# Performance work log

Measured on AMD Instinct MI355X. Metric: run time of the kernel, lower is better.

## Reference

```python
import jax, jax.numpy as jnp
import numpy as np

M_DIM = 256  # attention key dim, used for 1/sqrt(M) scaling


def sparsemax(z):
    # z: [..., F]. Martins & Astudillo sparsemax along last axis.
    F = z.shape[-1]
    zs = -jnp.sort(-z, axis=-1)                      # sorted descending
    css = jnp.cumsum(zs, axis=-1)                    # cumulative sums
    r = jnp.arange(1, F + 1, dtype=z.dtype)
    support = zs * r > (css - 1.0)                   # k(z) condition
    k = jnp.sum(support, axis=-1, keepdims=True)     # support size >= 1
    css_k = jnp.take_along_axis(css, k.astype(jnp.int32) - 1, axis=-1)
    tau = (css_k - 1.0) / k.astype(z.dtype)          # threshold
    return jnp.maximum(z - tau, 0.0)


def setup_inputs() -> dict:
    key = jax.random.key(0)
    ks = jax.random.split(key, 5)
    B, D, F, M = 4096, 1024, 8192, M_DIM
    bound = 0.01
    x = jax.random.normal(ks[0], (B, D), dtype=jnp.float32)
    X_data = jax.random.normal(ks[1], (F, D), dtype=jnp.float32)
    Wq = jax.random.uniform(ks[2], (M, D), dtype=jnp.float32, minval=-bound, maxval=bound)
    Wk = jax.random.uniform(ks[3], (M, D), dtype=jnp.float32, minval=-bound, maxval=bound)
    Wv = jax.random.uniform(ks[4], (D, D), dtype=jnp.float32, minval=-2 * bound, maxval=2 * bound)
    return {
        'x': x, 'X_data': X_data,
        'Wq': Wq, 'bq': jnp.zeros((M,), jnp.float32),
        'Wk': Wk, 'bk': jnp.zeros((M,), jnp.float32),
        'Wv': Wv, 'bv': jnp.zeros((D,), jnp.float32),
    }


def reference(x, X_data, Wq, bq, Wk, bk, Wv, bv):
    M = Wq.shape[0]
    scale = 1.0 / jnp.sqrt(jnp.asarray(M, x.dtype))
    Q = (x @ Wq.T + bq) * scale            # [B, M]
    K = (X_data @ Wk.T + bk) * scale       # [F, M]
    V = X_data @ Wv.T + bv                 # [F, D]
    scores = Q @ K.T                       # [B, F]  (note: 1/M total scaling, as in source)
    attn = sparsemax(scores)               # [B, F], sparse simplex projection
    x_hat = attn @ V                       # [B, D]
    return (x, x_hat, attn)
```

## Files before the change

kernel.cpp:

```cpp
#include <hip/hip_runtime.h>
#include <cstdint>
#include <cstddef>

typedef __attribute__((ext_vector_type(4))) float f32x4;
typedef __attribute__((ext_vector_type(8))) short bf16x8;
typedef __attribute__((ext_vector_type(4))) unsigned short u16x4;
typedef __attribute__((ext_vector_type(8))) unsigned short u16x8;

#define GPTR(p) ((const __attribute__((address_space(1))) void*)(p))
#define LPTR(p) ((__attribute__((address_space(3))) void*)(p))

static constexpr int BB = 4096;
static constexpr int DD = 1024;
static constexpr int FF = 8192;
static constexpr int MM = 256;

__device__ __forceinline__ unsigned short f2bf(float f) {
    union { float f; unsigned u; } x; x.f = f;
    return (unsigned short)((x.u + 0x7FFFu + ((x.u >> 16) & 1u)) >> 16);
}
__device__ __forceinline__ float bf2f(unsigned short h) {
    union { unsigned u; float f; } x; x.u = ((unsigned)h) << 16;
    return x.f;
}
__device__ __forceinline__ int xcd_swz(int bid, int grid) {
    const int cpx = grid >> 3;
    return (bid & 7) * cpx + (bid >> 3);
}

__global__ __launch_bounds__(256) void cvt_all(
    const float* __restrict__ x,  const float* __restrict__ Xd,
    const float* __restrict__ Wq, const float* __restrict__ Wk, const float* __restrict__ Wv,
    float* __restrict__ out_x,
    unsigned short* __restrict__ xb,  unsigned short* __restrict__ Xb,
    unsigned short* __restrict__ Wqb, unsigned short* __restrict__ Wkb, unsigned short* __restrict__ Wvb)
{
    constexpr int S0 = BB * DD;
    constexpr int S1 = FF * DD;
    constexpr int SW = MM * DD;
    const int i = (blockIdx.x * 256 + threadIdx.x) * 4;
    if (i < S0) {
        f32x4 v = *(const f32x4*)(x + i);
        *(f32x4*)(out_x + i) = v;
        u16x4 o; o.x = f2bf(v.x); o.y = f2bf(v.y); o.z = f2bf(v.z); o.w = f2bf(v.w);
        *(u16x4*)(xb + i) = o;
    } else if (i < S0 + S1) {
        const int j = i - S0;
        f32x4 v = *(const f32x4*)(Xd + j);
        u16x4 o; o.x = f2bf(v.x); o.y = f2bf(v.y); o.z = f2bf(v.z); o.w = f2bf(v.w);
        *(u16x4*)(Xb + j) = o;
    } else {
        int j = i - S0 - S1;
        const float* in; unsigned short* outp;
        if (j < SW)            { in = Wq; outp = Wqb; }
        else if (j < 2 * SW)   { in = Wk; outp = Wkb; j -= SW; }
        else                   { in = Wv; outp = Wvb; j -= 2 * SW; }
        f32x4 v = *(const f32x4*)(in + j);
        u16x4 o; o.x = f2bf(v.x); o.y = f2bf(v.y); o.z = f2bf(v.z); o.w = f2bf(v.w);
        *(u16x4*)(outp + j) = o;
    }
}

template<int Mo, int No, int Kd, int BIAS_MODE>
__device__ __forceinline__ void gemm128_core(
    const unsigned short* __restrict__ A,
    const unsigned short* __restrict__ Bm,
    unsigned short* __restrict__ Out,
    const float* __restrict__ bias, float scale,
    int L, unsigned short* As, unsigned short* Bs)
{
    constexpr int mt = Mo >> 7, nt = No >> 7;
    const int tid  = threadIdx.x;
    const int lane = tid & 63;
    const int wid  = tid >> 6;
    const int tm = (L % mt) << 7;
    const int tn = ((L / mt) % nt) << 7;
    const int wm = (wid >> 1) * 64;
    const int wn = (wid & 1) * 64;
    const int lr = lane & 15;
    const int lg = lane >> 4;

    f32x4 acc[4][4] = {};

    const unsigned short* aptr = A  + (size_t)(tm + (tid >> 2)) * Kd + ((tid & 3) << 3);
    const unsigned short* bptr = Bm + (size_t)(tn + (tid >> 2)) * Kd + ((tid & 3) << 3);
    unsigned short* As_base = &As[wid * 512];
    unsigned short* Bs_base = &Bs[wid * 512];

    for (int k0 = 0; k0 < Kd; k0 += 32) {
        __builtin_amdgcn_global_load_lds(GPTR(aptr + k0),                   LPTR(As_base),        16, 0, 0);
        __builtin_amdgcn_global_load_lds(GPTR(aptr + (size_t)64 * Kd + k0), LPTR(As_base + 2048), 16, 0, 0);
        __builtin_amdgcn_global_load_lds(GPTR(bptr + k0),                   LPTR(Bs_base),        16, 0, 0);
        __builtin_amdgcn_global_load_lds(GPTR(bptr + (size_t)64 * Kd + k0), LPTR(Bs_base + 2048), 16, 0, 0);
        __syncthreads();

        bf16x8 af[4], bfr[4];
        #pragma unroll
        for (int mi = 0; mi < 4; ++mi)
            af[mi] = *(const bf16x8*)&As[(wm + mi * 16 + lr) * 32 + lg * 8];
        #pragma unroll
        for (int ni = 0; ni < 4; ++ni)
            bfr[ni] = *(const bf16x8*)&Bs[(wn + ni * 16 + lr) * 32 + lg * 8];

        #pragma unroll
        for (int mi = 0; mi < 4; ++mi)
            #pragma unroll
            for (int ni = 0; ni < 4; ++ni)
                acc[mi][ni] = __builtin_amdgcn_mfma_f32_16x16x32_bf16(af[mi], bfr[ni], acc[mi][ni], 0, 0, 0);
        __syncthreads();
    }

    #pragma unroll
    for (int mi = 0; mi < 4; ++mi)
        #pragma unroll
        for (int ni = 0; ni < 4; ++ni)
            #pragma unroll
            for (int r = 0; r < 4; ++r) {
                const int row = tm + wm + mi * 16 + lg * 4 + r;
                const int col = tn + wn + ni * 16 + lr;
                float v = acc[mi][ni][r];
                if (BIAS_MODE == 1) v = (v + bias[col]) * scale;
                if (BIAS_MODE == 2) v = v + bias[row];
                Out[(size_t)row * No + col] = f2bf(v);
            }
}

__global__ __launch_bounds__(256) void proj_all(
    const unsigned short* __restrict__ xb,  const unsigned short* __restrict__ Xb,
    const unsigned short* __restrict__ Wqb, const unsigned short* __restrict__ Wkb,
    const unsigned short* __restrict__ Wvb,
    unsigned short* __restrict__ Qb, unsigned short* __restrict__ Kb, unsigned short* __restrict__ Vtb,
    const float* __restrict__ bq, const float* __restrict__ bk, const float* __restrict__ bv,
    float scl)
{
    __shared__ alignas(16) unsigned short As[128 * 32];
    __shared__ alignas(16) unsigned short Bs[128 * 32];
    const int bid = blockIdx.x;
    if (bid < 512) {
        gemm128_core<DD, FF, DD, 2>(Wvb, Xb, Vtb, bv, 1.0f, xcd_swz(bid, 512), As, Bs);
    } else if (bid < 640) {
        gemm128_core<FF, MM, DD, 1>(Xb, Wkb, Kb, bk, scl, xcd_swz(bid - 512, 128), As, Bs);
    } else {
        gemm128_core<BB, MM, DD, 1>(xb, Wqb, Qb, bq, scl, xcd_swz(bid - 640, 64), As, Bs);
    }
}

template<int Mo, int No, int Kd, int KC, int DIRECT>
__global__ __launch_bounds__(512) void gemm256(
    const unsigned short* __restrict__ A,
    const unsigned short* __restrict__ Bm,
    unsigned short* __restrict__ Out)
{
    constexpr int KCH = Kd / KC;
    constexpr int NT  = KCH / 32;
    constexpr int mt  = Mo >> 8;
    constexpr int nt  = No >> 8;

    __shared__ alignas(16) unsigned short SH[4 * 16384];

    const int tid  = threadIdx.x;
    const int lane = tid & 63;
    const int wid  = tid >> 6;
    const int wr   = wid >> 2;
    const int wc   = wid & 3;
    const int lr   = lane & 15;
    const int lg   = lane >> 4;

    const int L  = xcd_swz(blockIdx.x, KC * mt * nt);
    const int tn = (L % nt) << 8;
    const int r0 = L / nt;
    const int tm = (r0 % mt) << 8;
    const int kc = r0 / mt;
    const size_t kbase = (size_t)kc * KCH;

    const unsigned short* ag0 = A  + (size_t)(tm + (tid >> 2)) * Kd + kbase + ((tid & 3) << 3);
    const unsigned short* bg0 = Bm + (size_t)(tn + (tid >> 2)) * Kd + kbase + ((tid & 3) << 3);

    auto STAGE_A = [&](int tt) {
        const int buf = tt & 3;
        #pragma unroll
        for (int s = 0; s < 2; ++s)
            __builtin_amdgcn_global_load_lds(GPTR(ag0 + (size_t)(s * 128) * Kd + tt * 32),
                LPTR(&SH[buf * 16384 + s * 4096 + wid * 512]), 16, 0, 0);
    };
    auto STAGE_B = [&](int tt) {
        const int buf = tt & 3;
        #pragma unroll
        for (int s = 0; s < 2; ++s)
            __builtin_amdgcn_global_load_lds(GPTR(bg0 + (size_t)(s * 128) * Kd + tt * 32),
                LPTR(&SH[buf * 16384 + 8192 + s * 4096 + wid * 512]), 16, 0, 0);
    };

    f32x4 acc[8][4] = {};

    STAGE_A(0); STAGE_B(0);
    STAGE_A(1); STAGE_B(1);
    STAGE_A(2); STAGE_B(2);
    asm volatile("s_waitcnt vmcnt(8)" ::: "memory");
    __builtin_amdgcn_s_barrier();

    #pragma unroll 1
    for (int t = 0; t < NT; ++t) {
        if (t) {
            if (t < NT - 2)      asm volatile("s_waitcnt vmcnt(8)" ::: "memory");
            else if (t == NT-2)  asm volatile("s_waitcnt vmcnt(4)" ::: "memory");
            else                 asm volatile("s_waitcnt vmcnt(0)" ::: "memory");
            __builtin_amdgcn_s_barrier();
        }
        const int buf = t & 3;
        const unsigned short* Ab = &SH[buf * 16384];
        const unsigned short* Bb = &SH[buf * 16384 + 8192];

        bf16x8 bfr[4], af[4];
        #pragma unroll
        for (int ni = 0; ni < 4; ++ni)
            bfr[ni] = *(const bf16x8*)&Bb[(wc * 64 + ni * 16 + lr) * 32 + lg * 8];
        #pragma unroll
        for (int mi = 0; mi < 4; ++mi)
            af[mi] = *(const bf16x8*)&Ab[(wr * 128 + mi * 16 + lr) * 32 + lg * 8];
        if (t + 3 < NT) STAGE_A(t + 3);
        __builtin_amdgcn_sched_barrier(0);
        __builtin_amdgcn_s_setprio(1);
        #pragma unroll
        for (int mi = 0; mi < 4; ++mi)
            #pragma unroll
            for (int ni = 0; ni < 4; ++ni)
                acc[mi][ni] = __builtin_amdgcn_mfma_f32_16x16x32_bf16(af[mi], bfr[ni], acc[mi][ni], 0, 0, 0);
        __builtin_amdgcn_s_setprio(0);
        __builtin_amdgcn_s_barrier();

        bf16x8 af2[4];
        #pragma unroll
        for (int mi = 0; mi < 4; ++mi)
            af2[mi] = *(const bf16x8*)&Ab[(wr * 128 + 64 + mi * 16 + lr) * 32 + lg * 8];
        if (t + 3 < NT) STAGE_B(t + 3);
        __builtin_amdgcn_sched_barrier(0);
        __builtin_amdgcn_s_setprio(1);
        #pragma unroll
        for (int mi = 0; mi < 4; ++mi)
            #pragma unroll
            for (int ni = 0; ni < 4; ++ni)
                acc[4 + mi][ni] = __builtin_amdgcn_mfma_f32_16x16x32_bf16(af2[mi], bfr[ni], acc[4 + mi][ni], 0, 0, 0);
        __builtin_amdgcn_s_setprio(0);
    }

    unsigned short* Ok = DIRECT ? (Out + (size_t)tm * No + tn)
                                : (Out + ((size_t)kc * Mo + tm) * No + tn);
    #pragma unroll
    for (int mi = 0; mi < 8; ++mi)
        #pragma unroll
        for (int ni = 0; ni < 4; ++ni)
            #pragma unroll
            for (int r = 0; r < 4; ++r) {
                const int row = wr * 128 + mi * 16 + lg * 4 + r;
                const int col = wc * 64 + ni * 16 + lr;
                Ok[(size_t)row * No + col] = f2bf(acc[mi][ni][r]);
            }
}

template<int KC>
__global__ __launch_bounds__(256) void reduce_sk(
    const unsigned short* __restrict__ P, float* __restrict__ out, size_t total)
{
    const size_t i = ((size_t)blockIdx.x * 256 + threadIdx.x) * 8;
    float v[8] = {0,0,0,0,0,0,0,0};
    #pragma unroll
    for (int kc = 0; kc < KC; ++kc) {
        u16x8 p = *(const u16x8*)(P + kc * total + i);
        #pragma unroll
        for (int c = 0; c < 8; ++c) v[c] += bf2f(p[c]);
    }
    f32x4 o0, o1;
    #pragma unroll
    for (int c = 0; c < 4; ++c) { o0[c] = v[c]; o1[c] = v[4 + c]; }
    *(f32x4*)(out + i)     = o0;
    *(f32x4*)(out + i + 4) = o1;
}

__global__ __launch_bounds__(256) void sparsemax_k(unsigned short* __restrict__ SA,
                                                   float* __restrict__ attn)
{
    __shared__ float red[16];
    const int t = threadIdx.x;
    const int w = t >> 6, lane = t & 63;
    unsigned short* Zrow = SA + (size_t)blockIdx.x * FF;
    float* Arow = attn + (size_t)blockIdx.x * FF;

    f32x4 z[8];
    #pragma unroll
    for (int j = 0; j < 4; ++j) {
        u16x8 v = *(const u16x8*)&Zrow[j * 2048 + t * 8];
        #pragma unroll
        for (int c = 0; c < 4; ++c) {
            z[2 * j][c]     = bf2f(v[c]);
            z[2 * j + 1][c] = bf2f(v[4 + c]);
        }
    }

    float mx = -1e30f, sm = 0.0f;
    #pragma unroll
    for (int j = 0; j < 8; ++j)
        #pragma unroll
        for (int c = 0; c < 4; ++c) { mx = fmaxf(mx, z[j][c]); sm += z[j][c]; }
    #pragma unroll
    for (int off = 32; off > 0; off >>= 1) {
        mx = fmaxf(mx, __shfl_xor(mx, off));
        sm += __shfl_xor(sm, off);
    }
    if (lane == 0) { red[w] = mx; red[8 + w] = sm; }
    __syncthreads();
    mx = fmaxf(fmaxf(red[0], red[1]), fmaxf(red[2], red[3]));
    sm = red[8] + red[9] + red[10] + red[11];
    __syncthreads();

    float lo = fmaxf(mx - 1.0f, (sm - 1.0f) * (1.0f / (float)FF));
    float hi = mx - 1.0f / (float)FF;

    for (int it = 0; it < 8; ++it) {
        const float mid = 0.5f * (lo + hi);
        float s = 0.0f;
        #pragma unroll
        for (int j = 0; j < 8; ++j)
            #pragma unroll
            for (int c = 0; c < 4; ++c) s += fmaxf(z[j][c] - mid, 0.0f);
        #pragma unroll
        for (int off = 32; off > 0; off >>= 1) s += __shfl_xor(s, off);
        if (lane == 0) red[w] = s;
        __syncthreads();
        s = red[0] + red[1] + red[2] + red[3];
        __syncthreads();
        if (s >= 1.0f) lo = mid; else hi = mid;
    }

    for (int it = 0; it < 2; ++it) {
        float s = 0.0f, cnt = 0.0f;
        #pragma unroll
        for (int j = 0; j < 8; ++j)
            #pragma unroll
            for (int c = 0; c < 4; ++c) {
                const float v = z[j][c];
                if (v > lo) { s += v; cnt += 1.0f; }
            }
        #pragma unroll
        for (int off = 32; off > 0; off >>= 1) { s += __shfl_xor(s, off); cnt += __shfl_xor(cnt, off); }
        if (lane == 0) { red[w] = s; red[8 + w] = cnt; }
        __syncthreads();
        s   = red[0] + red[1] + red[2] + red[3];
        cnt = red[8] + red[9] + red[10] + red[11];
        __syncthreads();
        lo = (s - 1.0f) / cnt;
    }
    const float tau = lo;

    #pragma unroll
    for (int j = 0; j < 4; ++j) {
        f32x4 a0, a1;
        #pragma unroll
        for (int c = 0; c < 4; ++c) {
            a0[c] = fmaxf(z[2 * j][c] - tau, 0.0f);
            a1[c] = fmaxf(z[2 * j + 1][c] - tau, 0.0f);
        }
        *(f32x4*)&Arow[j * 2048 + t * 8]     = a0;
        *(f32x4*)&Arow[j * 2048 + t * 8 + 4] = a1;
        u16x8 o;
        #pragma unroll
        for (int c = 0; c < 4; ++c) { o[c] = f2bf(a0[c]); o[4 + c] = f2bf(a1[c]); }
        *(u16x8*)&Zrow[j * 2048 + t * 8] = o;
    }
}

extern "C" void kernel_launch(void* const* d_in, const int* in_sizes, int n_in,
                              void* d_out, int out_size, void* d_ws, size_t ws_size,
                              hipStream_t stream) {
    const float* x  = (const float*)d_in[0];
    const float* Xd = (const float*)d_in[1];
    const float* Wq = (const float*)d_in[2];
    const float* bq = (const float*)d_in[3];
    const float* Wk = (const float*)d_in[4];
    const float* bk = (const float*)d_in[5];
    const float* Wv = (const float*)d_in[6];
    const float* bv = (const float*)d_in[7];

    float* out       = (float*)d_out;
    float* out_xhat  = out + (size_t)BB * DD;
    float* out_attn  = out + (size_t)2 * BB * DD;

    char* w = (char*)d_ws;
    unsigned short* xb  = (unsigned short*)w; w += (size_t)BB * DD * 2;
    unsigned short* Xb  = (unsigned short*)w; w += (size_t)FF * DD * 2;
    unsigned short* Wqb = (unsigned short*)w; w += (size_t)MM * DD * 2;
    unsigned short* Wkb = (unsigned short*)w; w += (size_t)MM * DD * 2;
    unsigned short* Wvb = (unsigned short*)w; w += (size_t)DD * DD * 2;
    unsigned short* Qb  = (unsigned short*)w; w += (size_t)BB * MM * 2;
    unsigned short* Kb  = (unsigned short*)w; w += (size_t)FF * MM * 2;
    unsigned short* Vtb = (unsigned short*)w; w += (size_t)DD * FF * 2;
    unsigned short* Sb  = (unsigned short*)w; w += (size_t)BB * FF * 2;

    unsigned short* Pb = (unsigned short*)d_ws;

    constexpr int CVT_N = BB * DD + FF * DD + 2 * MM * DD + DD * DD;
    cvt_all<<<CVT_N / 1024, 256, 0, stream>>>(x, Xd, Wq, Wk, Wv, out, xb, Xb, Wqb, Wkb, Wvb);

    proj_all<<<704, 256, 0, stream>>>(xb, Xb, Wqb, Wkb, Wvb, Qb, Kb, Vtb, bq, bk, bv, 0.0625f);

    gemm256<BB, FF, MM, 1, 1><<<(BB/256) * (FF/256), 512, 0, stream>>>(Qb, Kb, Sb);

    sparsemax_k<<<BB, 256, 0, stream>>>(Sb, out_attn);

    gemm256<BB, DD, FF, 4, 0><<<4 * (BB/256) * (DD/256), 512, 0, stream>>>(Sb, Vtb, Pb);

    reduce_sk<4><<<BB * DD / 2048, 256, 0, stream>>>(Pb, out_xhat, (size_t)BB * DD);
}
```

Baseline: 214.7 us.

## Co-schedule V projection GEMM with sparsemax in one launch

Moves the V projection GEMM out of the initial projection launch and fuses it into the same grid as the row-wise sparsemax, so the compute-bound GEMM blocks and the memory-bound sparsemax blocks can run concurrently on the GPU. The Q/K projection launch shrinks to 192 blocks, so the scores GEMM can start earlier. The fused kernel carries both the GEMM shared-memory footprint and the reduction buffer, and the small Q/K launch may underfill the device.

```diff
diff --git a/kernel.cpp b/kernel.cpp
--- a/kernel.cpp
+++ b/kernel.cpp
@@ -125,23 +125,125 @@
             }
 }
 
-__global__ __launch_bounds__(256) void proj_all(
+__global__ __launch_bounds__(256) void proj_qk(
     const unsigned short* __restrict__ xb,  const unsigned short* __restrict__ Xb,
     const unsigned short* __restrict__ Wqb, const unsigned short* __restrict__ Wkb,
-    const unsigned short* __restrict__ Wvb,
-    unsigned short* __restrict__ Qb, unsigned short* __restrict__ Kb, unsigned short* __restrict__ Vtb,
-    const float* __restrict__ bq, const float* __restrict__ bk, const float* __restrict__ bv,
-    float scl)
+    unsigned short* __restrict__ Qb, unsigned short* __restrict__ Kb,
+    const float* __restrict__ bq, const float* __restrict__ bk, float scl)
 {
     __shared__ alignas(16) unsigned short As[128 * 32];
     __shared__ alignas(16) unsigned short Bs[128 * 32];
     const int bid = blockIdx.x;
+    if (bid < 128) {
+        gemm128_core<FF, MM, DD, 1>(Xb, Wkb, Kb, bk, scl, xcd_swz(bid, 128), As, Bs);
+    } else {
+        gemm128_core<BB, MM, DD, 1>(xb, Wqb, Qb, bq, scl, xcd_swz(bid - 128, 64), As, Bs);
+    }
+}
+
+__device__ __forceinline__ void sparsemax_row(unsigned short* __restrict__ Zrow,
+                                              float* __restrict__ Arow, float* red)
+{
+    const int t = threadIdx.x;
+    const int w = t >> 6, lane = t & 63;
+
+    f32x4 z[8];
+    #pragma unroll
+    for (int j = 0; j < 4; ++j) {
+        u16x8 v = *(const u16x8*)&Zrow[j * 2048 + t * 8];
+        #pragma unroll
+        for (int c = 0; c < 4; ++c) {
+            z[2 * j][c]     = bf2f(v[c]);
+            z[2 * j + 1][c] = bf2f(v[4 + c]);
+        }
+    }
+
+    float mx = -1e30f, sm = 0.0f;
+    #pragma unroll
+    for (int j = 0; j < 8; ++j)
+        #pragma unroll
+        for (int c = 0; c < 4; ++c) { mx = fmaxf(mx, z[j][c]); sm += z[j][c]; }
+    #pragma unroll
+    for (int off = 32; off > 0; off >>= 1) {
+        mx = fmaxf(mx, __shfl_xor(mx, off));
+        sm += __shfl_xor(sm, off);
+    }
+    if (lane == 0) { red[w] = mx; red[8 + w] = sm; }
+    __syncthreads();
+    mx = fmaxf(fmaxf(red[0], red[1]), fmaxf(red[2], red[3]));
+    sm = red[8] + red[9] + red[10] + red[11];
+    __syncthreads();
+
+    float lo = fmaxf(mx - 1.0f, (sm - 1.0f) * (1.0f / (float)FF));
+    float hi = mx - 1.0f / (float)FF;
+
+    for (int it = 0; it < 8; ++it) {
+        const float mid = 0.5f * (lo + hi);
+        float s = 0.0f;
+        #pragma unroll
+        for (int j = 0; j < 8; ++j)
+            #pragma unroll
+            for (int c = 0; c < 4; ++c) s += fmaxf(z[j][c] - mid, 0.0f);
+        #pragma unroll
+        for (int off = 32; off > 0; off >>= 1) s += __shfl_xor(s, off);
+        if (lane == 0) red[w] = s;
+        __syncthreads();
+        s = red[0] + red[1] + red[2] + red[3];
+        __syncthreads();
+        if (s >= 1.0f) lo = mid; else hi = mid;
+    }
+
+    for (int it = 0; it < 2; ++it) {
+        float s = 0.0f, cnt = 0.0f;
+        #pragma unroll
+        for (int j = 0; j < 8; ++j)
+            #pragma unroll
+            for (int c = 0; c < 4; ++c) {
+                const float v = z[j][c];
+                if (v > lo) { s += v; cnt += 1.0f; }
+            }
+        #pragma unroll
+        for (int off = 32; off > 0; off >>= 1) { s += __shfl_xor(s, off); cnt += __shfl_xor(cnt, off); }
+        if (lane == 0) { red[w] = s; red[8 + w] = cnt; }
+        __syncthreads();
+        s   = red[0] + red[1] + red[2] + red[3];
+        cnt = red[8] + red[9] + red[10] + red[11];
+        __syncthreads();
+        lo = (s - 1.0f) / cnt;
+    }
+    const float tau = lo;
+
+    #pragma unroll
+    for (int j = 0; j < 4; ++j) {
+        f32x4 a0, a1;
+        #pragma unroll
+        for (int c = 0; c < 4; ++c) {
+            a0[c] = fmaxf(z[2 * j][c] - tau, 0.0f);
+            a1[c] = fmaxf(z[2 * j + 1][c] - tau, 0.0f);
+        }
+        *(f32x4*)&Arow[j * 2048 + t * 8]     = a0;
+        *(f32x4*)&Arow[j * 2048 + t * 8 + 4] = a1;
+        u16x8 o;
+        #pragma unroll
+        for (int c = 0; c < 4; ++c) { o[c] = f2bf(a0[c]); o[4 + c] = f2bf(a1[c]); }
+        *(u16x8*)&Zrow[j * 2048 + t * 8] = o;
+    }
+}
+
+__global__ __launch_bounds__(256) void sm_vt(
+    const unsigned short* __restrict__ Wvb, const unsigned short* __restrict__ Xb,
+    unsigned short* __restrict__ Vtb, const float* __restrict__ bv,
+    unsigned short* __restrict__ SA, float* __restrict__ attn)
+{
+    __shared__ alignas(16) unsigned short As[128 * 32];
+    __shared__ alignas(16) unsigned short Bs[128 * 32];
+    __shared__ float red[16];
+    const int bid = blockIdx.x;
     if (bid < 512) {
         gemm128_core<DD, FF, DD, 2>(Wvb, Xb, Vtb, bv, 1.0f, xcd_swz(bid, 512), As, Bs);
-    } else if (bid < 640) {
-        gemm128_core<FF, MM, DD, 1>(Xb, Wkb, Kb, bk, scl, xcd_swz(bid - 512, 128), As, Bs);
     } else {
-        gemm128_core<BB, MM, DD, 1>(xb, Wqb, Qb, bq, scl, xcd_swz(bid - 640, 64), As, Bs);
+        const int row = bid - 512;
+        sparsemax_row(SA + (size_t)row * FF, attn + (size_t)row * FF, red);
     }
 }
 
@@ -277,98 +379,6 @@
     *(f32x4*)(out + i + 4) = o1;
 }
 
-__global__ __launch_bounds__(256) void sparsemax_k(unsigned short* __restrict__ SA,
-                                                   float* __restrict__ attn)
-{
-    __shared__ float red[16];
-    const int t = threadIdx.x;
-    const int w = t >> 6, lane = t & 63;
-    unsigned short* Zrow = SA + (size_t)blockIdx.x * FF;
-    float* Arow = attn + (size_t)blockIdx.x * FF;
-
-    f32x4 z[8];
-    #pragma unroll
-    for (int j = 0; j < 4; ++j) {
-        u16x8 v = *(const u16x8*)&Zrow[j * 2048 + t * 8];
-        #pragma unroll
-        for (int c = 0; c < 4; ++c) {
-            z[2 * j][c]     = bf2f(v[c]);
-            z[2 * j + 1][c] = bf2f(v[4 + c]);
-        }
-    }
-
-    float mx = -1e30f, sm = 0.0f;
-    #pragma unroll
-    for (int j = 0; j < 8; ++j)
-        #pragma unroll
-        for (int c = 0; c < 4; ++c) { mx = fmaxf(mx, z[j][c]); sm += z[j][c]; }
-    #pragma unroll
-    for (int off = 32; off > 0; off >>= 1) {
-        mx = fmaxf(mx, __shfl_xor(mx, off));
-        sm += __shfl_xor(sm, off);
-    }
-    if (lane == 0) { red[w] = mx; red[8 + w] = sm; }
-    __syncthreads();
-    mx = fmaxf(fmaxf(red[0], red[1]), fmaxf(red[2], red[3]));
-    sm = red[8] + red[9] + red[10] + red[11];
-    __syncthreads();
-
-    float lo = fmaxf(mx - 1.0f, (sm - 1.0f) * (1.0f / (float)FF));
-    float hi = mx - 1.0f / (float)FF;
-
-    for (int it = 0; it < 8; ++it) {
-        const float mid = 0.5f * (lo + hi);
-        float s = 0.0f;
-        #pragma unroll
-        for (int j = 0; j < 8; ++j)
-            #pragma unroll
-            for (int c = 0; c < 4; ++c) s += fmaxf(z[j][c] - mid, 0.0f);
-        #pragma unroll
-        for (int off = 32; off > 0; off >>= 1) s += __shfl_xor(s, off);
-        if (lane == 0) red[w] = s;
-        __syncthreads();
-        s = red[0] + red[1] + red[2] + red[3];
-        __syncthreads();
-        if (s >= 1.0f) lo = mid; else hi = mid;
-    }
-
-    for (int it = 0; it < 2; ++it) {
-        float s = 0.0f, cnt = 0.0f;
-        #pragma unroll
-        for (int j = 0; j < 8; ++j)
-            #pragma unroll
-            for (int c = 0; c < 4; ++c) {
-                const float v = z[j][c];
-                if (v > lo) { s += v; cnt += 1.0f; }
-            }
-        #pragma unroll
-        for (int off = 32; off > 0; off >>= 1) { s += __shfl_xor(s, off); cnt += __shfl_xor(cnt, off); }
-        if (lane == 0) { red[w] = s; red[8 + w] = cnt; }
-        __syncthreads();
-        s   = red[0] + red[1] + red[2] + red[3];
-        cnt = red[8] + red[9] + red[10] + red[11];
-        __syncthreads();
-        lo = (s - 1.0f) / cnt;
-    }
-    const float tau = lo;
-
-    #pragma unroll
-    for (int j = 0; j < 4; ++j) {
-        f32x4 a0, a1;
-        #pragma unroll
-        for (int c = 0; c < 4; ++c) {
-            a0[c] = fmaxf(z[2 * j][c] - tau, 0.0f);
-            a1[c] = fmaxf(z[2 * j + 1][c] - tau, 0.0f);
-        }
-        *(f32x4*)&Arow[j * 2048 + t * 8]     = a0;
-        *(f32x4*)&Arow[j * 2048 + t * 8 + 4] = a1;
-        u16x8 o;
-        #pragma unroll
-        for (int c = 0; c < 4; ++c) { o[c] = f2bf(a0[c]); o[4 + c] = f2bf(a1[c]); }
-        *(u16x8*)&Zrow[j * 2048 + t * 8] = o;
-    }
-}
-
 extern "C" void kernel_launch(void* const* d_in, const int* in_sizes, int n_in,
                               void* d_out, int out_size, void* d_ws, size_t ws_size,
                               hipStream_t stream) {
@@ -401,11 +411,11 @@
     constexpr int CVT_N = BB * DD + FF * DD + 2 * MM * DD + DD * DD;
     cvt_all<<<CVT_N / 1024, 256, 0, stream>>>(x, Xd, Wq, Wk, Wv, out, xb, Xb, Wqb, Wkb, Wvb);
 
-    proj_all<<<704, 256, 0, stream>>>(xb, Xb, Wqb, Wkb, Wvb, Qb, Kb, Vtb, bq, bk, bv, 0.0625f);
+    proj_qk<<<192, 256, 0, stream>>>(xb, Xb, Wqb, Wkb, Qb, Kb, bq, bk, 0.0625f);
 
     gemm256<BB, FF, MM, 1, 1><<<(BB/256) * (FF/256), 512, 0, stream>>>(Qb, Kb, Sb);
 
-    sparsemax_k<<<BB, 256, 0, stream>>>(Sb, out_attn);
+    sm_vt<<<512 + BB, 256, 0, stream>>>(Wvb, Xb, Vtb, bv, Sb, out_attn);
 
     gemm256<BB, DD, FF, 4, 0><<<4 * (BB/256) * (DD/256), 512, 0, stream>>>(Sb, Vtb, Pb);
 
```

New measurement: 234.5 us. 9.2% more time.
